# Optimization experiments

Measured on AMD Instinct MI355X. Metric: run time of the kernel, lower is better.

## Reference

```python
import jax, jax.numpy as jnp
import numpy as np

N = 100000
E = 1600000
IN_C = 256
HID = 256
OUT_C = 32
K = 2          # APPNP K = max(1, num_layers)
ALPHA = 0.1


def setup_inputs() -> dict:
    key = jax.random.key(0)
    ks = jax.random.split(key, 8)
    x = jax.random.normal(ks[0], (N, IN_C), dtype=jnp.float32)
    edge_index = jax.random.randint(ks[1], (2, E), 0, N, dtype=jnp.int64)
    s_in = 1.0 / np.sqrt(IN_C)
    s_h = 1.0 / np.sqrt(HID)
    W_in = jax.random.uniform(ks[2], (IN_C, HID), jnp.float32, -s_in, s_in)
    b_in = jax.random.uniform(ks[3], (HID,), jnp.float32, -s_in, s_in)
    W_h = jax.random.uniform(ks[4], (HID, HID), jnp.float32, -s_h, s_h)
    b_h = jax.random.uniform(ks[5], (HID,), jnp.float32, -s_h, s_h)
    W_out = jax.random.uniform(ks[6], (HID, OUT_C), jnp.float32, -s_h, s_h)
    b_out = jax.random.uniform(ks[7], (OUT_C,), jnp.float32, -s_h, s_h)
    return {"x": x, "edge_index": edge_index, "W_in": W_in, "b_in": b_in,
            "W_h": W_h, "b_h": b_h, "W_out": W_out, "b_out": b_out}


def _appnp(h0, src, dst):
    # gcn_norm with added self-loops: deg over destinations, sym normalization
    loops = jnp.arange(N, dtype=src.dtype)
    src_f = jnp.concatenate([src, loops])  # [E+N]
    dst_f = jnp.concatenate([dst, loops])
    deg = jax.ops.segment_sum(jnp.ones_like(dst_f, dtype=h0.dtype), dst_f,
                              num_segments=N)
    dinv = jnp.where(deg > 0, jax.lax.rsqrt(jnp.maximum(deg, 1e-12)), 0.0)
    norm = (dinv[src_f] * dinv[dst_f])[:, None]  # [E+N, 1]
    h = h0
    for _ in range(K):
        agg = jax.ops.segment_sum(h[src_f] * norm, dst_f, num_segments=N)
        h = (1.0 - ALPHA) * agg + ALPHA * h0
    return h


def reference(x, edge_index, W_in, b_in, W_h, b_h, W_out, b_out):
    # MLP encoder (dropout inactive in eval mode)
    h = jax.nn.relu(x @ W_in + b_in)
    h = jax.nn.relu(h @ W_h + b_h)
    h = h @ W_out + b_out  # [N, OUT_C]
    return _appnp(h, edge_index[0], edge_index[1])
```

## Files before the change

### kernel.cpp

```cpp
#include <hip/hip_runtime.h>

#define NN 100000
#define NE 1600000
#define NT64 1563
#define SCALE_BLKS 1563

#define BSH 7
#define BNODES 128
#define NBUCK 782
#define NBUCKP 784
#define CAP 2560
#define ECH 8192
#define NCHK 196
#define WFRAG_BLKS 272

typedef _Float16 half8v __attribute__((ext_vector_type(8)));
typedef _Float16 half4v __attribute__((ext_vector_type(4)));
typedef float f32x4 __attribute__((ext_vector_type(4)));


__device__ __forceinline__ void wfrag_one(const float* __restrict__ W,
                                          _Float16* __restrict__ Wf, int idx, int N) {
    int j = idx & 7;
    int l = (idx >> 3) & 63;
    int f = idx >> 9;
    int nt = f % (N / 16);
    int kt = f / (N / 16);
    int k = kt * 32 + (l >> 4) * 8 + j;
    int c = nt * 16 + (l & 15);
    Wf[idx] = (_Float16)W[k * N + c];
}


__global__ __launch_bounds__(512) void k_count_wfrag(const int* __restrict__ dst,
                                                     int* __restrict__ histT,
                                                     const float* __restrict__ W1,
                                                     const float* __restrict__ W2,
                                                     const float* __restrict__ W3,
                                                     _Float16* __restrict__ Wf1,
                                                     _Float16* __restrict__ Wf2,
                                                     _Float16* __restrict__ Wf3) {
    const int t = threadIdx.x;
    if (blockIdx.x >= NCHK) {
        int idx = (blockIdx.x - NCHK) * 512 + t;
        if (idx < 65536) wfrag_one(W1, Wf1, idx, 256);
        else if (idx < 131072) wfrag_one(W2, Wf2, idx - 65536, 256);
        else if (idx < 139264) wfrag_one(W3, Wf3, idx - 131072, 32);
        return;
    }
    __shared__ int h[NBUCKP];
    const int blk = blockIdx.x;
    for (int b = t; b < NBUCKP; b += 512) h[b] = 0;
    __syncthreads();
    const int ebase = blk * ECH + t * 16;
#pragma unroll
    for (int q = 0; q < 4; q++) {
        int e = ebase + q * 4;
        if (e + 4 <= NE) {
            int4 d4 = *reinterpret_cast<const int4*>(dst + e);
            atomicAdd(&h[d4.x >> BSH], 1);
            atomicAdd(&h[d4.y >> BSH], 1);
            atomicAdd(&h[d4.z >> BSH], 1);
            atomicAdd(&h[d4.w >> BSH], 1);
        } else {
            for (int p = e; p < NE; p++) atomicAdd(&h[dst[p] >> BSH], 1);
            break;
        }
    }
    __syncthreads();
    for (int b = t; b < NBUCK; b += 512) histT[(long long)b * NCHK + blk] = h[b];
}


__global__ __launch_bounds__(256) void k_scanb(int* __restrict__ histT,
                                               int* __restrict__ cntb) {
    __shared__ int s[256];
    const int b = blockIdx.x, t = threadIdx.x;
    int* row = histT + (long long)b * NCHK;
    int v = (t < NCHK) ? row[t] : 0;
    s[t] = v;
    __syncthreads();
    for (int off = 1; off < 256; off <<= 1) {
        int u = (t >= off) ? s[t - off] : 0;
        __syncthreads();
        s[t] += u;
        __syncthreads();
    }
    if (t < NCHK) row[t] = s[t] - v;
    if (t == 255) cntb[b] = s[255];
}


__global__ __launch_bounds__(512) void k_part_mlp(const int* __restrict__ src,
                                                  const int* __restrict__ dst,
                                                  const int* __restrict__ histT,
                                                  int* __restrict__ data,
                                                  const float* __restrict__ x,
                                                  const _Float16* __restrict__ Wf1,
                                                  const _Float16* __restrict__ Wf2,
                                                  const _Float16* __restrict__ Wf3,
                                                  const float* __restrict__ b1,
                                                  const float* __restrict__ b2,
                                                  const float* __restrict__ b3,
                                                  _Float16* __restrict__ h0f) {
    __shared__ char smem[32768];
    const int t = threadIdx.x;

    if (blockIdx.x < NCHK) {
        int* curs = (int*)smem;
        const int blk = blockIdx.x;
        for (int b = t; b < NBUCKP; b += 512)
            curs[b] = b * CAP + ((b < NBUCK) ? histT[(long long)b * NCHK + blk] : 0);
        __syncthreads();
        const int ebase = blk * ECH + t * 16;
#pragma unroll
        for (int q = 0; q < 4; q++) {
            int e = ebase + q * 4;
            if (e + 4 <= NE) {
                int4 d4 = *reinterpret_cast<const int4*>(dst + e);
                int4 s4 = *reinterpret_cast<const int4*>(src + e);
                int p0 = atomicAdd(&curs[d4.x >> BSH], 1);
                data[p0] = (s4.x << BSH) | (d4.x & (BNODES - 1));
                int p1 = atomicAdd(&curs[d4.y >> BSH], 1);
                data[p1] = (s4.y << BSH) | (d4.y & (BNODES - 1));
                int p2 = atomicAdd(&curs[d4.z >> BSH], 1);
                data[p2] = (s4.z << BSH) | (d4.z & (BNODES - 1));
                int p3 = atomicAdd(&curs[d4.w >> BSH], 1);
                data[p3] = (s4.w << BSH) | (d4.w & (BNODES - 1));
            } else {
                for (int p = e; p < NE; p++) {
                    int d = dst[p], sv = src[p];
                    int pos = atomicAdd(&curs[d >> BSH], 1);
                    data[pos] = (sv << BSH) | (d & (BNODES - 1));
                }
                break;
            }
        }
        return;
    }

    char* buf = smem;
    const int lane = t & 63;
    const int G = lane >> 4;
    const int w = t >> 6;
    const int T = blockIdx.x - NCHK;
    const long long row0 = (long long)T * 64;

    const half8v* W1f = reinterpret_cast<const half8v*>(Wf1);
    const half8v* W2f = reinterpret_cast<const half8v*>(Wf2);
    float bv1[2], bv2[2];
#pragma unroll
    for (int n2 = 0; n2 < 2; n2++) {
        bv1[n2] = b1[w * 32 + n2 * 16 + (lane & 15)];
        bv2[n2] = b2[w * 32 + n2 * 16 + (lane & 15)];
    }

    {
        const float4* A4 = reinterpret_cast<const float4*>(x + row0 * 256);
        float4 v[8];
#pragma unroll
        for (int q = 0; q < 8; q++) {
            int i = t + q * 512;
            int r = i >> 6;
            v[q] = make_float4(0.f, 0.f, 0.f, 0.f);
            if (row0 + r < NN) v[q] = A4[i];
        }
        __builtin_amdgcn_sched_barrier(0);
#pragma unroll
        for (int q = 0; q < 8; q++) {
            int i = t + q * 512;
            int r = i >> 6, c4 = i & 63;
            half4v hv;
            hv[0] = (_Float16)v[q].x; hv[1] = (_Float16)v[q].y;
            hv[2] = (_Float16)v[q].z; hv[3] = (_Float16)v[q].w;
            int bo = (r * 512 + c4 * 8) ^ ((r & 7) << 4);
            *reinterpret_cast<half4v*>(buf + bo) = hv;
        }
    }
    __syncthreads();

    f32x4 acc[4][2];

#pragma unroll
    for (int mt = 0; mt < 4; mt++)
#pragma unroll
        for (int n2 = 0; n2 < 2; n2++) acc[mt][n2] = (f32x4)0.f;
#pragma unroll
    for (int kt = 0; kt < 8; kt++) {
        half8v a[4], bfr[2];
#pragma unroll
        for (int n2 = 0; n2 < 2; n2++)
            bfr[n2] = W1f[(kt * 16 + 2 * w + n2) * 64 + lane];
#pragma unroll
        for (int mt = 0; mt < 4; mt++) {
            int row = mt * 16 + (lane & 15);
            int bo = (row * 512 + kt * 64 + (G << 4)) ^ ((row & 7) << 4);
            a[mt] = *reinterpret_cast<const half8v*>(buf + bo);
        }
#pragma unroll
        for (int mt = 0; mt < 4; mt++)
#pragma unroll
            for (int n2 = 0; n2 < 2; n2++)
                acc[mt][n2] = __builtin_amdgcn_mfma_f32_16x16x32_f16(a[mt], bfr[n2], acc[mt][n2], 0, 0, 0);
    }
    __syncthreads();

#pragma unroll
    for (int mt = 0; mt < 4; mt++)
#pragma unroll
        for (int n2 = 0; n2 < 2; n2++) {
            int colc = w * 32 + n2 * 16 + (lane & 15);
            float bb = bv1[n2];
#pragma unroll
            for (int r = 0; r < 4; r++) {
                int row = mt * 16 + G * 4 + r;
                float v = fmaxf(acc[mt][n2][r] + bb, 0.f);
                int bo = (row * 512 + colc * 2) ^ ((row & 7) << 4);
                *reinterpret_cast<_Float16*>(buf + bo) = (_Float16)v;
            }
        }
    __syncthreads();

#pragma unroll
    for (int mt = 0; mt < 4; mt++)
#pragma unroll
        for (int n2 = 0; n2 < 2; n2++) acc[mt][n2] = (f32x4)0.f;
#pragma unroll
    for (int kt = 0; kt < 8; kt++) {
        half8v a[4], bfr[2];
#pragma unroll
        for (int n2 = 0; n2 < 2; n2++)
            bfr[n2] = W2f[(kt * 16 + 2 * w + n2) * 64 + lane];
#pragma unroll
        for (int mt = 0; mt < 4; mt++) {
            int row = mt * 16 + (lane & 15);
            int bo = (row * 512 + kt * 64 + (G << 4)) ^ ((row & 7) << 4);
            a[mt] = *reinterpret_cast<const half8v*>(buf + bo);
        }
#pragma unroll
        for (int mt = 0; mt < 4; mt++)
#pragma unroll
            for (int n2 = 0; n2 < 2; n2++)
                acc[mt][n2] = __builtin_amdgcn_mfma_f32_16x16x32_f16(a[mt], bfr[n2], acc[mt][n2], 0, 0, 0);
    }
    __syncthreads();

#pragma unroll
    for (int mt = 0; mt < 4; mt++)
#pragma unroll
        for (int n2 = 0; n2 < 2; n2++) {
            int colc = w * 32 + n2 * 16 + (lane & 15);
            float bb = bv2[n2];
#pragma unroll
            for (int r = 0; r < 4; r++) {
                int row = mt * 16 + G * 4 + r;
                float v = fmaxf(acc[mt][n2][r] + bb, 0.f);
                int bo = (row * 512 + colc * 2) ^ ((row & 7) << 4);
                *reinterpret_cast<_Float16*>(buf + bo) = (_Float16)v;
            }
        }
    __syncthreads();

    {
        const half8v* W3f = reinterpret_cast<const half8v*>(Wf3);
        const int mt3 = w >> 1, ct3 = w & 1;
        const float bb3 = b3[ct3 * 16 + (lane & 15)];
        f32x4 a3 = (f32x4)0.f;
#pragma unroll
        for (int kt = 0; kt < 8; kt++) {
            int row = mt3 * 16 + (lane & 15);
            int bo = (row * 512 + kt * 64 + (G << 4)) ^ ((row & 7) << 4);
            half8v a = *reinterpret_cast<const half8v*>(buf + bo);
            half8v b = W3f[(kt * 2 + ct3) * 64 + lane];
            a3 = __builtin_amdgcn_mfma_f32_16x16x32_f16(a, b, a3, 0, 0, 0);
        }
        int colc = ct3 * 16 + (lane & 15);
#pragma unroll
        for (int r = 0; r < 4; r++) {
            long long row = row0 + mt3 * 16 + G * 4 + r;
            if (row < NN) h0f[row * 32 + colc] = (_Float16)(a3[r] + bb3);
        }
    }
}


__global__ __launch_bounds__(256) void k_deg(const int* __restrict__ data,
                                             const int* __restrict__ cntb,
                                             float* __restrict__ dinv) {
    __shared__ int c[BNODES];
    const int b = blockIdx.x, t = threadIdx.x;
    if (t < BNODES) c[t] = 0;
    __syncthreads();
    const int cnt = cntb[b];
    const int* wp = data + b * CAP;
    for (int e = t; e < cnt; e += 256) atomicAdd(&c[wp[e] & (BNODES - 1)], 1);
    __syncthreads();
    int node = (b << BSH) + t;
    if (t < BNODES && node < NN) dinv[node] = rsqrtf((float)(c[t] + 1));
}


__global__ __launch_bounds__(256) void k_sortb_scale(const int* __restrict__ data,
                                                     const int* __restrict__ cntb,
                                                     int* __restrict__ col,
                                                     int* __restrict__ begp,
                                                     int* __restrict__ endp,
                                                     const float* __restrict__ dinv,
                                                     const _Float16* __restrict__ h0f,
                                                     _Float16* __restrict__ hs0) {
    const int t = threadIdx.x;
    if (blockIdx.x >= NBUCK) {
        int idx = (blockIdx.x - NBUCK) * 256 + t;
        if (idx < NN * 4) {
            int node = idx >> 2;
            float dd = dinv[node];
            half8v v = *reinterpret_cast<const half8v*>(h0f + (size_t)idx * 8);
            half8v o;
#pragma unroll
            for (int j = 0; j < 8; j++) o[j] = (_Float16)(dd * (float)v[j]);
            *reinterpret_cast<half8v*>(hs0 + (size_t)idx * 8) = o;
        }
        return;
    }
    __shared__ int hist[BNODES];
    __shared__ int scn[BNODES];
    __shared__ int curs[BNODES];
    const int b = blockIdx.x;
    if (t < BNODES) hist[t] = 0;
    __syncthreads();
    const int cnt = cntb[b];
    const int* wp = data + b * CAP;
    for (int e = t; e < cnt; e += 256) atomicAdd(&hist[wp[e] & (BNODES - 1)], 1);
    __syncthreads();
    if (t < BNODES) scn[t] = hist[t];
    __syncthreads();
    for (int off = 1; off < BNODES; off <<= 1) {
        int v = (t < BNODES && t >= off) ? scn[t - off] : 0;
        __syncthreads();
        if (t < BNODES) scn[t] += v;
        __syncthreads();
    }
    if (t < BNODES) {
        int beg = scn[t] - hist[t];
        curs[t] = beg;
        int node = (b << BSH) + t;
        if (node < NN) {
            begp[node] = b * CAP + beg;
            endp[node] = b * CAP + scn[t];
        }
    }
    __syncthreads();
    for (int e = t; e < cnt; e += 256) {
        int w = wp[e];
        int p = atomicAdd(&curs[w & (BNODES - 1)], 1);
        col[b * CAP + p] = w >> BSH;
    }
}


template<bool FINAL>
__global__ __launch_bounds__(256) void k_appnp(const int* __restrict__ begp,
                                               const int* __restrict__ endp,
                                               const int* __restrict__ col,
                                               const float* __restrict__ dinv,
                                               const _Float16* __restrict__ hs,
                                               const _Float16* __restrict__ h0f,
                                               void* __restrict__ outp) {
    int node = blockIdx.x * 4 + (threadIdx.x >> 6);
    if (node >= NN) return;
    const int lane = threadIdx.x & 63;
    const int slot = lane >> 2;
    const int cg = lane & 3;

    const int beg = begp[node];
    const int end = endp[node];
    const float dd = dinv[node];
    const half8v selfv = *reinterpret_cast<const half8v*>(hs + (size_t)node * 32 + cg * 8);
    const half8v h0v = *reinterpret_cast<const half8v*>(h0f + (size_t)node * 32 + cg * 8);

    float acc[8];
#pragma unroll
    for (int j = 0; j < 8; j++) acc[j] = 0.f;

    for (int e = beg + slot; e < end; e += 16) {
        int s = col[e];
        half8v v = *reinterpret_cast<const half8v*>(hs + (size_t)s * 32 + cg * 8);
#pragma unroll
        for (int j = 0; j < 8; j++) acc[j] += (float)v[j];
    }

#pragma unroll
    for (int off = 4; off < 64; off <<= 1) {
#pragma unroll
        for (int j = 0; j < 8; j++) acc[j] += __shfl_xor(acc[j], off, 64);
    }

    if (slot == 0) {
        float o[8];
#pragma unroll
        for (int j = 0; j < 8; j++)
            o[j] = 0.9f * dd * (acc[j] + (float)selfv[j]) + 0.1f * (float)h0v[j];
        size_t off = (size_t)node * 32 + cg * 8;
        if (FINAL) {
            float4 v0 = make_float4(o[0], o[1], o[2], o[3]);
            float4 v1 = make_float4(o[4], o[5], o[6], o[7]);
            float4* op = reinterpret_cast<float4*>((float*)outp + off);
            op[0] = v0; op[1] = v1;
        } else {
            half8v hv;
#pragma unroll
            for (int j = 0; j < 8; j++) hv[j] = (_Float16)(dd * o[j]);
            *reinterpret_cast<half8v*>((_Float16*)outp + off) = hv;
        }
    }
}


extern "C" void kernel_launch(void* const* d_in, const int* in_sizes, int n_in,
                              void* d_out, int out_size, void* d_ws, size_t ws_size,
                              hipStream_t stream) {
    const float* x     = (const float*)d_in[0];
    const int*   ei    = (const int*)d_in[1];
    const float* W_in  = (const float*)d_in[2];
    const float* b_in  = (const float*)d_in[3];
    const float* W_h   = (const float*)d_in[4];
    const float* b_h   = (const float*)d_in[5];
    const float* W_out = (const float*)d_in[6];
    const float* b_out = (const float*)d_in[7];
    float* out = (float*)d_out;

    const int* srcv = ei;
    const int* dstv = ei + NE;

    char* ws = (char*)d_ws;
    _Float16* h0f  = (_Float16*)ws;
    _Float16* hs0  = h0f + (size_t)NN * 32;
    _Float16* hs1  = hs0 + (size_t)NN * 32;
    float* dinv    = (float*)(hs1 + (size_t)NN * 32);
    _Float16* Wf_in  = (_Float16*)(dinv + NN);
    _Float16* Wf_h   = Wf_in + 256 * 256;
    _Float16* Wf_out = Wf_h + 256 * 256;
    int* histT = (int*)(Wf_out + 256 * 32);
    int* cntb  = histT + (size_t)NBUCK * NCHK;
    int* data  = cntb + NBUCKP;
    int* col   = data + (size_t)NBUCKP * CAP;
    int* begp  = col + (size_t)NBUCKP * CAP;
    int* endp  = begp + NN;

    k_count_wfrag<<<NCHK + WFRAG_BLKS, 512, 0, stream>>>(dstv, histT,
                                                         W_in, W_h, W_out,
                                                         Wf_in, Wf_h, Wf_out);
    k_scanb<<<NBUCK, 256, 0, stream>>>(histT, cntb);

    k_part_mlp<<<NCHK + NT64, 512, 0, stream>>>(srcv, dstv, histT, data,
                                                x, Wf_in, Wf_h, Wf_out,
                                                b_in, b_h, b_out, h0f);

    k_deg<<<NBUCK, 256, 0, stream>>>(data, cntb, dinv);

    k_sortb_scale<<<NBUCK + SCALE_BLKS, 256, 0, stream>>>(data, cntb, col, begp, endp,
                                                          dinv, h0f, hs0);

    k_appnp<false><<<(NN + 3) / 4, 256, 0, stream>>>(begp, endp, col, dinv, hs0, h0f, hs1);
    k_appnp<true ><<<(NN + 3) / 4, 256, 0, stream>>>(begp, endp, col, dinv, hs1, h0f, out);
}
```

Baseline: 155.0 us.

## Pre-convert x to swizzled fp16 image and load it via global_load_lds

Moves the fp32-to-fp16 conversion and LDS swizzle of x out of the MLP kernel into the first (count/weight-fragment) kernel, writing a pre-swizzled fp16 image to workspace. The MLP kernel then copies that image straight into LDS with global_load_lds, skipping register staging and conversion. This adds a full extra pass over x (read fp32, write fp16, read fp16 again), trading more total memory traffic for a leaner, possibly better-overlapped MLP prologue.

```diff
diff --git a/kernel.cpp b/kernel.cpp
--- a/kernel.cpp
+++ b/kernel.cpp
@@ -32,15 +32,36 @@
 }
 
 
-__global__ __launch_bounds__(512) void k_count_wfrag(const int* __restrict__ dst,
-                                                     int* __restrict__ histT,
-                                                     const float* __restrict__ W1,
-                                                     const float* __restrict__ W2,
-                                                     const float* __restrict__ W3,
-                                                     _Float16* __restrict__ Wf1,
-                                                     _Float16* __restrict__ Wf2,
-                                                     _Float16* __restrict__ Wf3) {
+__global__ __launch_bounds__(512) void k_cwx(const int* __restrict__ dst,
+                                             int* __restrict__ histT,
+                                             const float* __restrict__ W1,
+                                             const float* __restrict__ W2,
+                                             const float* __restrict__ W3,
+                                             _Float16* __restrict__ Wf1,
+                                             _Float16* __restrict__ Wf2,
+                                             _Float16* __restrict__ Wf3,
+                                             const float* __restrict__ x,
+                                             _Float16* __restrict__ x16) {
     const int t = threadIdx.x;
+    if (blockIdx.x >= NCHK + WFRAG_BLKS) {
+        const int T = blockIdx.x - NCHK - WFRAG_BLKS;
+        const long long row0 = (long long)T * 64;
+        const float4* A4 = reinterpret_cast<const float4*>(x + row0 * 256);
+        char* img = (char*)(x16 + (size_t)T * 16384);
+#pragma unroll
+        for (int q = 0; q < 8; q++) {
+            int i = t + q * 512;
+            int r = i >> 6, c4 = i & 63;
+            float4 v = make_float4(0.f, 0.f, 0.f, 0.f);
+            if (row0 + r < NN) v = A4[i];
+            half4v hv;
+            hv[0] = (_Float16)v.x; hv[1] = (_Float16)v.y;
+            hv[2] = (_Float16)v.z; hv[3] = (_Float16)v.w;
+            int bo = (r * 512 + c4 * 8) ^ ((r & 7) << 4);
+            *reinterpret_cast<half4v*>(img + bo) = hv;
+        }
+        return;
+    }
     if (blockIdx.x >= NCHK) {
         int idx = (blockIdx.x - NCHK) * 512 + t;
         if (idx < 65536) wfrag_one(W1, Wf1, idx, 256);
@@ -95,7 +116,7 @@
                                                   const int* __restrict__ dst,
                                                   const int* __restrict__ histT,
                                                   int* __restrict__ data,
-                                                  const float* __restrict__ x,
+                                                  const _Float16* __restrict__ x16,
                                                   const _Float16* __restrict__ Wf1,
                                                   const _Float16* __restrict__ Wf2,
                                                   const _Float16* __restrict__ Wf3,
@@ -156,25 +177,14 @@
     }
 
     {
-        const float4* A4 = reinterpret_cast<const float4*>(x + row0 * 256);
-        float4 v[8];
-#pragma unroll
-        for (int q = 0; q < 8; q++) {
-            int i = t + q * 512;
-            int r = i >> 6;
-            v[q] = make_float4(0.f, 0.f, 0.f, 0.f);
-            if (row0 + r < NN) v[q] = A4[i];
-        }
-        __builtin_amdgcn_sched_barrier(0);
-#pragma unroll
-        for (int q = 0; q < 8; q++) {
-            int i = t + q * 512;
-            int r = i >> 6, c4 = i & 63;
-            half4v hv;
-            hv[0] = (_Float16)v[q].x; hv[1] = (_Float16)v[q].y;
-            hv[2] = (_Float16)v[q].z; hv[3] = (_Float16)v[q].w;
-            int bo = (r * 512 + c4 * 8) ^ ((r & 7) << 4);
-            *reinterpret_cast<half4v*>(buf + bo) = hv;
+        const char* gsrc = (const char*)(x16 + (size_t)T * 16384) + w * 4096 + (lane << 4);
+        char* ldst = buf + w * 4096;
+#pragma unroll
+        for (int q = 0; q < 4; q++) {
+            __builtin_amdgcn_global_load_lds(
+                (const __attribute__((address_space(1))) void*)(gsrc + q * 1024),
+                (__attribute__((address_space(3))) void*)(ldst + q * 1024),
+                16, 0, 0);
         }
     }
     __syncthreads();
@@ -440,20 +450,22 @@
     _Float16* Wf_in  = (_Float16*)(dinv + NN);
     _Float16* Wf_h   = Wf_in + 256 * 256;
     _Float16* Wf_out = Wf_h + 256 * 256;
-    int* histT = (int*)(Wf_out + 256 * 32);
+    _Float16* x16    = Wf_out + 256 * 32;
+    int* histT = (int*)(x16 + (size_t)NT64 * 16384);
     int* cntb  = histT + (size_t)NBUCK * NCHK;
     int* data  = cntb + NBUCKP;
     int* col   = data + (size_t)NBUCKP * CAP;
     int* begp  = col + (size_t)NBUCKP * CAP;
     int* endp  = begp + NN;
 
-    k_count_wfrag<<<NCHK + WFRAG_BLKS, 512, 0, stream>>>(dstv, histT,
-                                                         W_in, W_h, W_out,
-                                                         Wf_in, Wf_h, Wf_out);
+    k_cwx<<<NCHK + WFRAG_BLKS + NT64, 512, 0, stream>>>(dstv, histT,
+                                                        W_in, W_h, W_out,
+                                                        Wf_in, Wf_h, Wf_out,
+                                                        x, x16);
     k_scanb<<<NBUCK, 256, 0, stream>>>(histT, cntb);
 
     k_part_mlp<<<NCHK + NT64, 512, 0, stream>>>(srcv, dstv, histT, data,
-                                                x, Wf_in, Wf_h, Wf_out,
+                                                x16, Wf_in, Wf_h, Wf_out,
                                                 b_in, b_h, b_out, h0f);
 
     k_deg<<<NBUCK, 256, 0, stream>>>(data, cntb, dinv);
```

Measured after the change: 168.2 us. +8.5%, slower.

## Pre-convert x to fp16 tiles, fold degree and pre-scale into sort/APPNP

Applied to the files above, without the earlier changes.

Adds an fp32-to-fp16 conversion of x into pre-swizzled 64-row tiles, run by extra blocks of the scan kernel. The MLP kernel then fills LDS from those tiles with direct global-to-LDS loads. Removes the separate degree kernel (dinv is now computed in the bucket sort) and the pre-scaling pass: the first APPNP layer reads unscaled h0 and multiplies each neighbour by dinv[s] on the fly. This trades two launches and a full-array scale pass for an extra fp16 round trip of x through memory and a per-edge dinv gather in layer one.

```diff
diff --git a/kernel.cpp b/kernel.cpp
--- a/kernel.cpp
+++ b/kernel.cpp
@@ -3,7 +3,6 @@
 #define NN 100000
 #define NE 1600000
 #define NT64 1563
-#define SCALE_BLKS 1563
 
 #define BSH 7
 #define BNODES 128
@@ -72,22 +71,45 @@
 }
 
 
-__global__ __launch_bounds__(256) void k_scanb(int* __restrict__ histT,
-                                               int* __restrict__ cntb) {
-    __shared__ int s[256];
-    const int b = blockIdx.x, t = threadIdx.x;
+__global__ __launch_bounds__(512) void k_scanb_xconv(int* __restrict__ histT,
+                                                     int* __restrict__ cntb,
+                                                     const float* __restrict__ x,
+                                                     _Float16* __restrict__ x16) {
+    const int t = threadIdx.x;
+    if (blockIdx.x >= NBUCK) {
+        const int T = blockIdx.x - NBUCK;
+        const long long row0 = (long long)T * 64;
+        const float4* A4 = reinterpret_cast<const float4*>(x + row0 * 256);
+        _Float16* tile = x16 + (size_t)T * 16384;
+#pragma unroll
+        for (int q = 0; q < 4; q++) {
+            int c = t + q * 512;
+            int r = c >> 5;
+            float4 lo = make_float4(0.f, 0.f, 0.f, 0.f), hi = lo;
+            if (row0 + r < NN) { lo = A4[c * 2]; hi = A4[c * 2 + 1]; }
+            half8v hv;
+            hv[0] = (_Float16)lo.x; hv[1] = (_Float16)lo.y;
+            hv[2] = (_Float16)lo.z; hv[3] = (_Float16)lo.w;
+            hv[4] = (_Float16)hi.x; hv[5] = (_Float16)hi.y;
+            hv[6] = (_Float16)hi.z; hv[7] = (_Float16)hi.w;
+            *reinterpret_cast<half8v*>(tile + c * 8) = hv;
+        }
+        return;
+    }
+    __shared__ int s[512];
+    const int b = blockIdx.x;
     int* row = histT + (long long)b * NCHK;
     int v = (t < NCHK) ? row[t] : 0;
     s[t] = v;
     __syncthreads();
-    for (int off = 1; off < 256; off <<= 1) {
+    for (int off = 1; off < 512; off <<= 1) {
         int u = (t >= off) ? s[t - off] : 0;
         __syncthreads();
         s[t] += u;
         __syncthreads();
     }
     if (t < NCHK) row[t] = s[t] - v;
-    if (t == 255) cntb[b] = s[255];
+    if (t == 511) cntb[b] = s[511];
 }
 
 
@@ -95,7 +117,7 @@
                                                   const int* __restrict__ dst,
                                                   const int* __restrict__ histT,
                                                   int* __restrict__ data,
-                                                  const float* __restrict__ x,
+                                                  const _Float16* __restrict__ x16,
                                                   const _Float16* __restrict__ Wf1,
                                                   const _Float16* __restrict__ Wf2,
                                                   const _Float16* __restrict__ Wf3,
@@ -156,25 +178,15 @@
     }
 
     {
-        const float4* A4 = reinterpret_cast<const float4*>(x + row0 * 256);
-        float4 v[8];
-#pragma unroll
-        for (int q = 0; q < 8; q++) {
-            int i = t + q * 512;
-            int r = i >> 6;
-            v[q] = make_float4(0.f, 0.f, 0.f, 0.f);
-            if (row0 + r < NN) v[q] = A4[i];
-        }
-        __builtin_amdgcn_sched_barrier(0);
-#pragma unroll
-        for (int q = 0; q < 8; q++) {
-            int i = t + q * 512;
-            int r = i >> 6, c4 = i & 63;
-            half4v hv;
-            hv[0] = (_Float16)v[q].x; hv[1] = (_Float16)v[q].y;
-            hv[2] = (_Float16)v[q].z; hv[3] = (_Float16)v[q].w;
-            int bo = (r * 512 + c4 * 8) ^ ((r & 7) << 4);
-            *reinterpret_cast<half4v*>(buf + bo) = hv;
+        const char* tile = (const char*)(x16 + (size_t)T * 16384);
+#pragma unroll
+        for (int q = 0; q < 4; q++) {
+            int CC = w * 256 + q * 64 + lane;
+            int scc = CC ^ ((CC >> 5) & 7);
+            __builtin_amdgcn_global_load_lds(
+                (const __attribute__((address_space(1))) void*)(tile + scc * 16),
+                (__attribute__((address_space(3))) void*)(buf + w * 4096 + q * 1024),
+                16, 0, 0);
         }
     }
     __syncthreads();
@@ -284,48 +296,16 @@
 }
 
 
-__global__ __launch_bounds__(256) void k_deg(const int* __restrict__ data,
-                                             const int* __restrict__ cntb,
-                                             float* __restrict__ dinv) {
-    __shared__ int c[BNODES];
-    const int b = blockIdx.x, t = threadIdx.x;
-    if (t < BNODES) c[t] = 0;
-    __syncthreads();
-    const int cnt = cntb[b];
-    const int* wp = data + b * CAP;
-    for (int e = t; e < cnt; e += 256) atomicAdd(&c[wp[e] & (BNODES - 1)], 1);
-    __syncthreads();
-    int node = (b << BSH) + t;
-    if (t < BNODES && node < NN) dinv[node] = rsqrtf((float)(c[t] + 1));
-}
-
-
-__global__ __launch_bounds__(256) void k_sortb_scale(const int* __restrict__ data,
-                                                     const int* __restrict__ cntb,
-                                                     int* __restrict__ col,
-                                                     int* __restrict__ begp,
-                                                     int* __restrict__ endp,
-                                                     const float* __restrict__ dinv,
-                                                     const _Float16* __restrict__ h0f,
-                                                     _Float16* __restrict__ hs0) {
-    const int t = threadIdx.x;
-    if (blockIdx.x >= NBUCK) {
-        int idx = (blockIdx.x - NBUCK) * 256 + t;
-        if (idx < NN * 4) {
-            int node = idx >> 2;
-            float dd = dinv[node];
-            half8v v = *reinterpret_cast<const half8v*>(h0f + (size_t)idx * 8);
-            half8v o;
-#pragma unroll
-            for (int j = 0; j < 8; j++) o[j] = (_Float16)(dd * (float)v[j]);
-            *reinterpret_cast<half8v*>(hs0 + (size_t)idx * 8) = o;
-        }
-        return;
-    }
+__global__ __launch_bounds__(256) void k_sortb(const int* __restrict__ data,
+                                               const int* __restrict__ cntb,
+                                               int* __restrict__ col,
+                                               int* __restrict__ begp,
+                                               int* __restrict__ endp,
+                                               float* __restrict__ dinv) {
     __shared__ int hist[BNODES];
     __shared__ int scn[BNODES];
     __shared__ int curs[BNODES];
-    const int b = blockIdx.x;
+    const int b = blockIdx.x, t = threadIdx.x;
     if (t < BNODES) hist[t] = 0;
     __syncthreads();
     const int cnt = cntb[b];
@@ -347,6 +327,7 @@
         if (node < NN) {
             begp[node] = b * CAP + beg;
             endp[node] = b * CAP + scn[t];
+            dinv[node] = rsqrtf((float)(hist[t] + 1));
         }
     }
     __syncthreads();
@@ -376,7 +357,6 @@
     const int end = endp[node];
     const float dd = dinv[node];
     const half8v selfv = *reinterpret_cast<const half8v*>(hs + (size_t)node * 32 + cg * 8);
-    const half8v h0v = *reinterpret_cast<const half8v*>(h0f + (size_t)node * 32 + cg * 8);
 
     float acc[8];
 #pragma unroll
@@ -385,8 +365,10 @@
     for (int e = beg + slot; e < end; e += 16) {
         int s = col[e];
         half8v v = *reinterpret_cast<const half8v*>(hs + (size_t)s * 32 + cg * 8);
-#pragma unroll
-        for (int j = 0; j < 8; j++) acc[j] += (float)v[j];
+        float sc = 1.f;
+        if (!FINAL) sc = dinv[s];
+#pragma unroll
+        for (int j = 0; j < 8; j++) acc[j] += sc * (float)v[j];
     }
 
 #pragma unroll
@@ -396,12 +378,13 @@
     }
 
     if (slot == 0) {
-        float o[8];
-#pragma unroll
-        for (int j = 0; j < 8; j++)
-            o[j] = 0.9f * dd * (acc[j] + (float)selfv[j]) + 0.1f * (float)h0v[j];
         size_t off = (size_t)node * 32 + cg * 8;
         if (FINAL) {
+            const half8v h0v = *reinterpret_cast<const half8v*>(h0f + off);
+            float o[8];
+#pragma unroll
+            for (int j = 0; j < 8; j++)
+                o[j] = 0.9f * dd * (acc[j] + (float)selfv[j]) + 0.1f * (float)h0v[j];
             float4 v0 = make_float4(o[0], o[1], o[2], o[3]);
             float4 v1 = make_float4(o[4], o[5], o[6], o[7]);
             float4* op = reinterpret_cast<float4*>((float*)outp + off);
@@ -409,7 +392,11 @@
         } else {
             half8v hv;
 #pragma unroll
-            for (int j = 0; j < 8; j++) hv[j] = (_Float16)(dd * o[j]);
+            for (int j = 0; j < 8; j++) {
+                float sv = (float)selfv[j];
+                float hnew = 0.9f * dd * (acc[j] + dd * sv) + 0.1f * sv;
+                hv[j] = (_Float16)(dd * hnew);
+            }
             *reinterpret_cast<half8v*>((_Float16*)outp + off) = hv;
         }
     }
@@ -434,13 +421,13 @@
 
     char* ws = (char*)d_ws;
     _Float16* h0f  = (_Float16*)ws;
-    _Float16* hs0  = h0f + (size_t)NN * 32;
-    _Float16* hs1  = hs0 + (size_t)NN * 32;
+    _Float16* hs1  = h0f + (size_t)NN * 32;
     float* dinv    = (float*)(hs1 + (size_t)NN * 32);
     _Float16* Wf_in  = (_Float16*)(dinv + NN);
     _Float16* Wf_h   = Wf_in + 256 * 256;
     _Float16* Wf_out = Wf_h + 256 * 256;
-    int* histT = (int*)(Wf_out + 256 * 32);
+    _Float16* x16    = Wf_out + 256 * 32;
+    int* histT = (int*)(x16 + (size_t)NT64 * 16384);
     int* cntb  = histT + (size_t)NBUCK * NCHK;
     int* data  = cntb + NBUCKP;
     int* col   = data + (size_t)NBUCKP * CAP;
@@ -450,17 +437,15 @@
     k_count_wfrag<<<NCHK + WFRAG_BLKS, 512, 0, stream>>>(dstv, histT,
                                                          W_in, W_h, W_out,
                                                          Wf_in, Wf_h, Wf_out);
-    k_scanb<<<NBUCK, 256, 0, stream>>>(histT, cntb);
+
+    k_scanb_xconv<<<NBUCK + NT64, 512, 0, stream>>>(histT, cntb, x, x16);
 
     k_part_mlp<<<NCHK + NT64, 512, 0, stream>>>(srcv, dstv, histT, data,
-                                                x, Wf_in, Wf_h, Wf_out,
+                                                x16, Wf_in, Wf_h, Wf_out,
                                                 b_in, b_h, b_out, h0f);
 
-    k_deg<<<NBUCK, 256, 0, stream>>>(data, cntb, dinv);
-
-    k_sortb_scale<<<NBUCK + SCALE_BLKS, 256, 0, stream>>>(data, cntb, col, begp, endp,
-                                                          dinv, h0f, hs0);
-
-    k_appnp<false><<<(NN + 3) / 4, 256, 0, stream>>>(begp, endp, col, dinv, hs0, h0f, hs1);
+    k_sortb<<<NBUCK, 256, 0, stream>>>(data, cntb, col, begp, endp, dinv);
+
+    k_appnp<false><<<(NN + 3) / 4, 256, 0, stream>>>(begp, endp, col, dinv, h0f, h0f, hs1);
     k_appnp<true ><<<(NN + 3) / 4, 256, 0, stream>>>(begp, endp, col, dinv, hs1, h0f, out);
 }
```

After: 167.5 us. +8.0%, slower.
